# Kernel tuning notes

Hardware: AMD Instinct MI355X
Metric: run time of the kernel (lower is better)

## Reference

```python
import jax, jax.numpy as jnp
import numpy as np

N = 100000   # nodes
E = 1200000  # edges
XD = 64      # x_dim
ED = 16      # edge_attr_dim
D = 64       # hidden_size
L = 3        # n_layers
G = 512      # num graphs
C = 10       # num_class
BN_EPS = 1e-5


def setup_inputs() -> dict:
    key = jax.random.key(0)
    ks = jax.random.split(key, 30)

    def w(k, shape, scale=0.05):
        return jax.random.normal(k, shape, jnp.float32) * scale

    inp = {
        "x": jax.random.normal(ks[0], (N, XD), jnp.float32),
        "edge_index": jax.random.randint(ks[1], (2, E), 0, N),
        "batch": jnp.sort(jax.random.randint(ks[2], (N,), 0, G)),
        "edge_attr": jax.random.normal(ks[3], (E, ED), jnp.float32),
        # encoders
        "w_node": w(ks[4], (XD, D)), "b_node": jnp.zeros((D,), jnp.float32),
        "w_edge": w(ks[5], (ED, D)), "b_edge": jnp.zeros((D,), jnp.float32),
        # per-layer GINEConv params (stacked over L layers)
        "lin_w": w(ks[6], (L, D, D)), "lin_b": jnp.zeros((L, D), jnp.float32),
        "mlp1_w": w(ks[7], (L, D, D)), "mlp1_b": jnp.zeros((L, D), jnp.float32),
        "bn1_g": jnp.ones((L, D), jnp.float32), "bn1_b": jnp.zeros((L, D), jnp.float32),
        "mlp2_w": w(ks[8], (L, D, D)), "mlp2_b": jnp.zeros((L, D), jnp.float32),
        # fc_out head: MLP(D,D) -> BN -> Linear(D,C)
        "fo1_w": w(ks[9], (D, D)), "fo1_b": jnp.zeros((D,), jnp.float32),
        "fo_bn1_g": jnp.ones((D,), jnp.float32), "fo_bn1_b": jnp.zeros((D,), jnp.float32),
        "fo2_w": w(ks[10], (D, D)), "fo2_b": jnp.zeros((D,), jnp.float32),
        "fo_bn2_g": jnp.ones((D,), jnp.float32), "fo_bn2_b": jnp.zeros((D,), jnp.float32),
        "fo3_w": w(ks[11], (D, C)), "fo3_b": jnp.zeros((C,), jnp.float32),
    }
    return inp


def _bn(h, g, b):
    # training-mode BatchNorm1d: biased variance over the batch dim
    mu = h.mean(0, keepdims=True)
    var = h.var(0, keepdims=True)
    return g * (h - mu) * (var + BN_EPS) ** -0.5 + b


def reference(x, edge_index, batch, edge_attr,
              w_node, b_node, w_edge, b_edge,
              lin_w, lin_b, mlp1_w, mlp1_b, bn1_g, bn1_b, mlp2_w, mlp2_b,
              fo1_w, fo1_b, fo_bn1_g, fo_bn1_b, fo2_w, fo2_b,
              fo_bn2_g, fo_bn2_b, fo3_w, fo3_b):
    src, dst = edge_index[0], edge_index[1]  # message flows src -> dst
    h = x @ w_node + b_node                  # [N, D]
    ea0 = edge_attr @ w_edge + b_edge        # [E, D] encoded edge features
    for l in range(L):
        ea = ea0 @ lin_w[l] + lin_b[l]                      # GINEConv.lin
        m = jax.nn.relu(h[src] + ea)                        # edge messages [E, D]
        agg = jax.ops.segment_sum(m, dst, num_segments=N)   # scatter-add
        h2 = agg + h                                        # + (1 + eps) * x_r, eps = 0
        h2 = h2 @ mlp1_w[l] + mlp1_b[l]
        h2 = jax.nn.relu(_bn(h2, bn1_g[l], bn1_b[l]))
        h2 = h2 @ mlp2_w[l] + mlp2_b[l]
        h = jax.nn.relu(h2)                                 # dropout is no-op at eval
    pooled = jax.ops.segment_sum(h, batch, num_segments=G)  # global_add_pool [G, D]
    g1 = pooled @ fo1_w + fo1_b
    g1 = jax.nn.relu(_bn(g1, fo_bn1_g, fo_bn1_b))
    g1 = g1 @ fo2_w + fo2_b
    g1 = _bn(g1, fo_bn2_g, fo_bn2_b)
    return g1 @ fo3_w + fo3_b                               # logits [G, C]
```

## Files before the change

kernel.cpp:

```cpp
#include <hip/hip_runtime.h>
#include <hip/hip_fp16.h>

#define NN 100000
#define NE 1200000
#define DD 64
#define EDIM 16
#define NL 3
#define NG 512
#define NC 10
#define NB_SCAN ((NN + 255) / 256)
#define EPW 32

typedef _Float16 f16x2 __attribute__((ext_vector_type(2)));
typedef _Float16 v8h   __attribute__((ext_vector_type(8)));
typedef float    v4f   __attribute__((ext_vector_type(4)));

__device__ __forceinline__ unsigned packh2(float a, float b) {
    f16x2 v; v[0] = (_Float16)a; v[1] = (_Float16)b;
    unsigned u; __builtin_memcpy(&u, &v, 4); return u;
}
__device__ __forceinline__ float dot2f(unsigned a, unsigned b, float c) {
    f16x2 av, bv;
    __builtin_memcpy(&av, &a, 4); __builtin_memcpy(&bv, &b, 4);
#if __has_builtin(__builtin_amdgcn_fdot2)
    return __builtin_amdgcn_fdot2(av, bv, c, false);
#else
    return c + (float)av[0]*(float)bv[0] + (float)av[1]*(float)bv[1];
#endif
}

__device__ __forceinline__ void atomic_pk_add_h2(_Float16* addr, float a, float b) {
    f16x2 v; v[0] = (_Float16)a; v[1] = (_Float16)b;
#if __has_builtin(__builtin_amdgcn_global_atomic_fadd_v2f16)
    typedef __attribute__((address_space(1))) f16x2 gh2;
    __builtin_amdgcn_global_atomic_fadd_v2f16((gh2*)addr, v);
#else
    unsigned* u = (unsigned*)addr;
    unsigned old = *u, assumed;
    do {
        assumed = old;
        f16x2 w; __builtin_memcpy(&w, &assumed, 4);
        w = w + v;
        unsigned nv; __builtin_memcpy(&nv, &w, 4);
        old = atomicCAS(u, assumed, nv);
    } while (old != assumed);
#endif
}

__global__ __launch_bounds__(1024) void prep_kernel(
    const float* __restrict__ w_edge, const float* __restrict__ b_edge,
    const float* __restrict__ lin_w, const float* __restrict__ lin_b,
    unsigned* __restrict__ Wc16, float* __restrict__ bc)
{
    __shared__ float sWc[1024];
    const int l = blockIdx.x;
    const int tid = threadIdx.x;
    const float* Lw = lin_w + l * 4096;
    const int k = tid >> 6, col = tid & 63;
    float acc = 0.f;
    for (int j = 0; j < 64; ++j) acc = fmaf(w_edge[k*64 + j], Lw[j*64 + col], acc);
    sWc[k*64 + col] = acc;
    if (tid < 64) {
        float a = lin_b[l*64 + tid];
        for (int j = 0; j < 64; ++j) a = fmaf(b_edge[j], Lw[j*64 + tid], a);
        bc[l*64 + tid] = a;
    }
    __syncthreads();
    if (tid < 512) {
        const int j = tid >> 6, c = tid & 63;
        Wc16[l*512 + j*64 + c] = packh2(sWc[(2*j)*64 + c], sWc[(2*j+1)*64 + c]);
    }
}

__global__ __launch_bounds__(512) void pack_w_kernel(
    const float* __restrict__ w_node, const float* __restrict__ mlp1_w,
    const float* __restrict__ mlp2_w, v8h* __restrict__ Wpk)
{
    const int m = blockIdx.x;
    const float* W = (m == 0) ? w_node
                   : (m <= 3) ? mlp1_w + (m-1)*4096
                              : mlp2_w + (m-4)*4096;
    const int fid = threadIdx.x >> 6;
    const int l   = threadIdx.x & 63;
    const int t = fid >> 1, f = fid & 1;
    const int n  = (l & 15) + 16*t;
    const int kb = f*32 + (l >> 4)*8;
    v8h v;
    #pragma unroll
    for (int j = 0; j < 8; ++j) v[j] = (_Float16)W[(kb + j)*64 + n];
    Wpk[m*512 + fid*64 + l] = v;
}

__global__ __launch_bounds__(256) void hist_kernel(
    const int* __restrict__ dst, int* __restrict__ counts)
{
    const int e = blockIdx.x * 256 + threadIdx.x;
    if (e < NE) atomicAdd(&counts[dst[e]], 1);
}

__global__ __launch_bounds__(256) void scan_reduce_kernel(
    const int* __restrict__ counts, int* __restrict__ bsum)
{
    __shared__ int sd[256];
    const int t = threadIdx.x;
    const int idx = blockIdx.x * 256 + t;
    sd[t] = (idx < NN) ? counts[idx] : 0;
    __syncthreads();
    for (int off = 128; off > 0; off >>= 1) {
        if (t < off) sd[t] += sd[t + off];
        __syncthreads();
    }
    if (t == 0) bsum[blockIdx.x] = sd[0];
}

__global__ __launch_bounds__(512) void scan_partials_kernel(
    const int* __restrict__ bsum, int* __restrict__ bscan)
{
    __shared__ int sd[512];
    const int t = threadIdx.x;
    sd[t] = (t < NB_SCAN) ? bsum[t] : 0;
    __syncthreads();
    for (int off = 1; off < 512; off <<= 1) {
        int u = (t >= off) ? sd[t - off] : 0;
        __syncthreads();
        sd[t] += u;
        __syncthreads();
    }
    if (t < NB_SCAN) bscan[t] = (t == 0) ? 0 : sd[t - 1];
}

__global__ __launch_bounds__(256) void scan_final_kernel(
    const int* __restrict__ counts, const int* __restrict__ bscan,
    int* __restrict__ rowptr, int* __restrict__ next)
{
    __shared__ int sd[256];
    const int t = threadIdx.x;
    const int idx = blockIdx.x * 256 + t;
    const int v = (idx < NN) ? counts[idx] : 0;
    sd[t] = v;
    __syncthreads();
    for (int off = 1; off < 256; off <<= 1) {
        int u = (t >= off) ? sd[t - off] : 0;
        __syncthreads();
        sd[t] += u;
        __syncthreads();
    }
    const int excl = sd[t] - v + bscan[blockIdx.x];
    if (idx < NN) { rowptr[idx] = excl; next[idx] = excl; }
    if (idx == NN - 1) rowptr[NN] = excl + v;
}

__global__ __launch_bounds__(256) void scatter_kernel(
    const int* __restrict__ src, const int* __restrict__ dst,
    const float* __restrict__ edge_attr,
    int* __restrict__ next, int* __restrict__ csr_src, uint4* __restrict__ csr_ea)
{
    const int e = blockIdx.x * 256 + threadIdx.x;
    if (e >= NE) return;
    const float4* q = (const float4*)(edge_attr + (size_t)e * 16);
    float4 a0 = q[0], a1 = q[1], a2 = q[2], a3 = q[3];
    const int pos = atomicAdd(&next[dst[e]], 1);
    csr_src[pos] = src[e];
    uint4 A, B;
    A.x = packh2(a0.x, a0.y); A.y = packh2(a0.z, a0.w);
    A.z = packh2(a1.x, a1.y); A.w = packh2(a1.z, a1.w);
    B.x = packh2(a2.x, a2.y); B.y = packh2(a2.z, a2.w);
    B.z = packh2(a3.x, a3.y); B.w = packh2(a3.z, a3.w);
    csr_ea[(size_t)pos*2 + 0] = A;
    csr_ea[(size_t)pos*2 + 1] = B;
}

__global__ __launch_bounds__(256) void agg_edge_kernel(
    const int* __restrict__ rowptr, const int* __restrict__ csr_src,
    const uint4* __restrict__ csr_ea,
    const unsigned* __restrict__ Wc16, const float* __restrict__ bc,
    const _Float16* __restrict__ h16, _Float16* __restrict__ agg16)
{
    __shared__ uint4 sEA[4][64];
    __shared__ int   sSRC[4][32];
    const int tid  = threadIdx.x;
    const int lane = tid & 63;
    const int wv   = tid >> 6;
    const int wid  = blockIdx.x * 4 + wv;
    const int e0   = wid * EPW;

    sEA[wv][lane] = csr_ea[(size_t)e0 * 2 + lane];
    if (lane < 32) sSRC[wv][lane] = csr_src[e0 + lane];

    unsigned wq[8];
    #pragma unroll
    for (int j = 0; j < 8; ++j) wq[j] = Wc16[j*64 + lane];
    const float mb = bc[lane];

    int lo = 0;
    {
        int idx = lane * 1563; if (idx > NN) idx = NN;
        lo += (__popcll(__ballot(rowptr[idx] <= e0)) - 1) * 1563;
        idx = lo + lane * 25; if (idx > NN) idx = NN;
        lo += (__popcll(__ballot(rowptr[idx] <= e0)) - 1) * 25;
        idx = lo + lane; if (idx > NN) idx = NN;
        lo += __popcll(__ballot(rowptr[idx] <= e0)) - 1;
    }
    int cur = lo;
    int nb  = rowptr[cur + 1];
    float acc = 0.f;

    __syncthreads();

    const uint4* eaw = sEA[wv];
    const int*   srw = sSRC[wv];

    auto msg = [&](uint4 A, uint4 B, float hv) -> float {
        float m = mb;
        m = dot2f(A.x, wq[0], m); m = dot2f(A.y, wq[1], m);
        m = dot2f(A.z, wq[2], m); m = dot2f(A.w, wq[3], m);
        m = dot2f(B.x, wq[4], m); m = dot2f(B.y, wq[5], m);
        m = dot2f(B.z, wq[6], m); m = dot2f(B.w, wq[7], m);
        return fmaxf(m + hv, 0.f);
    };
    auto flush = [&](int node, float v) {
        float other = __shfl_xor(v, 1);
        if ((lane & 1) == 0)
            atomic_pk_add_h2(agg16 + (size_t)node*64 + lane, v, other);
    };
    auto adv = [&](int q) {
        flush(cur, acc); acc = 0.f;
        do { ++cur; } while (rowptr[cur + 1] <= q);
        nb = rowptr[cur + 1];
    };
    auto doGroup = [&](int g, float hv0, float hv1, float hv2, float hv3) {
        const int p = e0 + g*4;
        float m0, m1, m2, m3;
        { uint4 A = eaw[g*8+0], B = eaw[g*8+1]; m0 = msg(A, B, hv0); }
        { uint4 A = eaw[g*8+2], B = eaw[g*8+3]; m1 = msg(A, B, hv1); }
        { uint4 A = eaw[g*8+4], B = eaw[g*8+5]; m2 = msg(A, B, hv2); }
        { uint4 A = eaw[g*8+6], B = eaw[g*8+7]; m3 = msg(A, B, hv3); }
        if (p + 3 < nb) {
            acc += (m0 + m1) + (m2 + m3);
        } else {
            if (p     >= nb) adv(p);     acc += m0;
            if (p + 1 >= nb) adv(p + 1); acc += m1;
            if (p + 2 >= nb) adv(p + 2); acc += m2;
            if (p + 3 >= nb) adv(p + 3); acc += m3;
        }
    };

    _Float16 a0, a1, a2, a3, b0, b1, b2, b3;
    {
        const int4 s = *(const int4*)&srw[0];
        a0 = h16[(size_t)s.x*64 + lane]; a1 = h16[(size_t)s.y*64 + lane];
        a2 = h16[(size_t)s.z*64 + lane]; a3 = h16[(size_t)s.w*64 + lane];
    }
    #pragma unroll 1
    for (int gp = 0; gp < EPW/8; ++gp) {
        const int g0 = gp*2, g1 = g0 + 1;
        {
            const int4 s = *(const int4*)&srw[g1*4];
            b0 = h16[(size_t)s.x*64 + lane]; b1 = h16[(size_t)s.y*64 + lane];
            b2 = h16[(size_t)s.z*64 + lane]; b3 = h16[(size_t)s.w*64 + lane];
        }
        doGroup(g0, (float)a0, (float)a1, (float)a2, (float)a3);
        if (gp + 1 < EPW/8) {
            const int4 s = *(const int4*)&srw[(g1 + 1)*4];
            a0 = h16[(size_t)s.x*64 + lane]; a1 = h16[(size_t)s.y*64 + lane];
            a2 = h16[(size_t)s.z*64 + lane]; a3 = h16[(size_t)s.w*64 + lane];
        }
        doGroup(g1, (float)b0, (float)b1, (float)b2, (float)b3);
    }
    flush(cur, acc);
}

template<bool IN_HALF, bool ADD_B, bool TRANS, bool OUT_RELU, bool OUT_ACCUM, bool OUT_F32, bool OUT_HALF>
__global__ __launch_bounds__(256) void mfma_gemm_kernel(
    const float* __restrict__ in0, const _Float16* __restrict__ in16,
    const _Float16* __restrict__ in16b,
    const v8h* __restrict__ Wpk, const float* __restrict__ bias,
    const float* __restrict__ scale, const float* __restrict__ shift,
    float* __restrict__ out, _Float16* __restrict__ out16,
    float* __restrict__ bn_sum, float* __restrict__ bn_sumsq)
{
    __shared__ float sS[1024];
    __shared__ float sQ[1024];
    const int tid = threadIdx.x;
    const int wv = tid >> 6, l = tid & 63;
    const int li = l & 15, quad = l >> 4;
    const int rb = (blockIdx.x * 4 + wv) * 16;
    const bool active = (rb < NN);

    v8h Bf[8];
    #pragma unroll
    for (int i = 0; i < 8; ++i) Bf[i] = Wpk[i*64 + l];

    v4f acc[4] = {v4f{0,0,0,0}, v4f{0,0,0,0}, v4f{0,0,0,0}, v4f{0,0,0,0}};

    if (active) {
        v8h Af[2];
        if constexpr (IN_HALF) {
            const size_t off = (size_t)(rb + li)*64 + quad*8;
            Af[0] = *(const v8h*)(in16 + off);
            Af[1] = *(const v8h*)(in16 + off + 32);
            if constexpr (ADD_B) {
                Af[0] += *(const v8h*)(in16b + off);
                Af[1] += *(const v8h*)(in16b + off + 32);
            }
        } else {
            const float* arow = in0 + (size_t)(rb + li)*64 + quad*8;
            #pragma unroll
            for (int f = 0; f < 2; ++f) {
                float4 x0 = *(const float4*)(arow + f*32);
                float4 x1 = *(const float4*)(arow + f*32 + 4);
                if constexpr (TRANS) {
                    const int kb = f*32 + quad*8;
                    float4 s0 = *(const float4*)(scale + kb);
                    float4 s1 = *(const float4*)(scale + kb + 4);
                    float4 t0 = *(const float4*)(shift + kb);
                    float4 t1 = *(const float4*)(shift + kb + 4);
                    x0.x = fmaxf(fmaf(x0.x, s0.x, t0.x), 0.f);
                    x0.y = fmaxf(fmaf(x0.y, s0.y, t0.y), 0.f);
                    x0.z = fmaxf(fmaf(x0.z, s0.z, t0.z), 0.f);
                    x0.w = fmaxf(fmaf(x0.w, s0.w, t0.w), 0.f);
                    x1.x = fmaxf(fmaf(x1.x, s1.x, t1.x), 0.f);
                    x1.y = fmaxf(fmaf(x1.y, s1.y, t1.y), 0.f);
                    x1.z = fmaxf(fmaf(x1.z, s1.z, t1.z), 0.f);
                    x1.w = fmaxf(fmaf(x1.w, s1.w, t1.w), 0.f);
                }
                v8h a;
                a[0] = (_Float16)x0.x; a[1] = (_Float16)x0.y;
                a[2] = (_Float16)x0.z; a[3] = (_Float16)x0.w;
                a[4] = (_Float16)x1.x; a[5] = (_Float16)x1.y;
                a[6] = (_Float16)x1.z; a[7] = (_Float16)x1.w;
                Af[f] = a;
            }
        }
        #pragma unroll
        for (int t = 0; t < 4; ++t) {
            acc[t] = __builtin_amdgcn_mfma_f32_16x16x32_f16(Af[0], Bf[t*2+0], acc[t], 0, 0, 0);
            acc[t] = __builtin_amdgcn_mfma_f32_16x16x32_f16(Af[1], Bf[t*2+1], acc[t], 0, 0, 0);
        }
    }

    float ps[4] = {0.f, 0.f, 0.f, 0.f}, pq[4] = {0.f, 0.f, 0.f, 0.f};
    if (active) {
        #pragma unroll
        for (int t = 0; t < 4; ++t) {
            const int col = li + 16*t;
            const float bcol = bias[col];
            #pragma unroll
            for (int r = 0; r < 4; ++r) {
                const int row = rb + quad*4 + r;
                float v = acc[t][r] + bcol;
                if constexpr (OUT_ACCUM) { ps[t] += v; pq[t] += v*v; }
                if constexpr (OUT_RELU) v = fmaxf(v, 0.f);
                if constexpr (OUT_F32)  out[(size_t)row*64 + col] = v;
                if constexpr (OUT_HALF) out16[(size_t)row*64 + col] = (_Float16)v;
            }
        }
    }

    if constexpr (OUT_ACCUM) {
        #pragma unroll
        for (int t = 0; t < 4; ++t) {
            sS[wv*256 + l*4 + t] = ps[t];
            sQ[wv*256 + l*4 + t] = pq[t];
        }
        __syncthreads();
        if (tid < 64) {
            const int t = tid >> 4, li2 = tid & 15;
            float s = 0.f, q = 0.f;
            #pragma unroll
            for (int w = 0; w < 4; ++w)
                #pragma unroll
                for (int qd = 0; qd < 4; ++qd) {
                    const int idx = w*256 + (qd*16 + li2)*4 + t;
                    s += sS[idx]; q += sQ[idx];
                }
            atomicAdd(bn_sum + tid, s);
            atomicAdd(bn_sumsq + tid, q);
        }
    }
}

template<int IN_MODE, bool OUT_RELU, bool OUT_ACCUM>
__global__ __launch_bounds__(256) void gemm64_kernel(
    const float* __restrict__ in0,
    const float* __restrict__ W, const float* __restrict__ bias,
    const float* __restrict__ scale, const float* __restrict__ shift,
    float* __restrict__ out, int nrows,
    float* __restrict__ bn_sum, float* __restrict__ bn_sumsq)
{
    __shared__ __align__(16) float sIn[64*64];
    __shared__ float sRedS[512];
    __shared__ float sRedQ[512];
    const int tid = threadIdx.x;
    const int c  = tid & 31;
    const int rg = tid >> 5;
    const int r0 = blockIdx.x * 64;

    float w0[64], w1[64];
    #pragma unroll
    for (int k = 0; k < 64; ++k) { w0[k] = W[k*64 + c]; w1[k] = W[k*64 + c + 32]; }
    const float b0 = bias[c], b1 = bias[c + 32];

    for (int i = tid; i < 1024; i += 256) {
        const int r  = i >> 4;
        const int c4 = (i & 15) * 4;
        const int gr = r0 + r;
        float4 v = make_float4(0.f, 0.f, 0.f, 0.f);
        if (gr < nrows) {
            v = *(const float4*)(in0 + (size_t)gr*64 + c4);
            if constexpr (IN_MODE == 2) {
                float4 s4 = *(const float4*)(scale + c4);
                float4 h4 = *(const float4*)(shift + c4);
                v.x = fmaxf(fmaf(v.x, s4.x, h4.x), 0.f);
                v.y = fmaxf(fmaf(v.y, s4.y, h4.y), 0.f);
                v.z = fmaxf(fmaf(v.z, s4.z, h4.z), 0.f);
                v.w = fmaxf(fmaf(v.w, s4.w, h4.w), 0.f);
            }
        }
        *(float4*)(sIn + r*64 + c4) = v;
    }
    __syncthreads();

    float ps0 = 0.f, psq0 = 0.f, ps1 = 0.f, psq1 = 0.f;
    #pragma unroll
    for (int i = 0; i < 8; ++i) {
        const int r = rg + 8*i;
        float a0 = b0, a1 = b1;
        #pragma unroll
        for (int k = 0; k < 64; k += 4) {
            float4 a = *(const float4*)(sIn + r*64 + k);
            a0 = fmaf(a.x, w0[k+0], a0); a1 = fmaf(a.x, w1[k+0], a1);
            a0 = fmaf(a.y, w0[k+1], a0); a1 = fmaf(a.y, w1[k+1], a1);
            a0 = fmaf(a.z, w0[k+2], a0); a1 = fmaf(a.z, w1[k+2], a1);
            a0 = fmaf(a.w, w0[k+3], a0); a1 = fmaf(a.w, w1[k+3], a1);
        }
        const int gr = r0 + r;
        if (gr < nrows) {
            if constexpr (OUT_ACCUM) {
                ps0 += a0; psq0 += a0*a0;
                ps1 += a1; psq1 += a1*a1;
            }
            out[(size_t)gr*64 + c]      = OUT_RELU ? fmaxf(a0, 0.f) : a0;
            out[(size_t)gr*64 + c + 32] = OUT_RELU ? fmaxf(a1, 0.f) : a1;
        }
    }

    if constexpr (OUT_ACCUM) {
        sRedS[rg*64 + c]      = ps0;
        sRedS[rg*64 + c + 32] = ps1;
        sRedQ[rg*64 + c]      = psq0;
        sRedQ[rg*64 + c + 32] = psq1;
        __syncthreads();
        if (tid < 64) {
            float s = 0.f, q = 0.f;
            #pragma unroll
            for (int g = 0; g < 8; ++g) { s += sRedS[g*64 + tid]; q += sRedQ[g*64 + tid]; }
            atomicAdd(bn_sum + tid, s);
            atomicAdd(bn_sumsq + tid, q);
        }
    }
}

__global__ __launch_bounds__(64) void bn_finalize_kernel(
    const float* __restrict__ sum, const float* __restrict__ sumsq,
    const float* __restrict__ gamma, const float* __restrict__ beta,
    float inv_count, float* __restrict__ scale, float* __restrict__ shift)
{
    const int t = threadIdx.x;
    float mu  = sum[t] * inv_count;
    float var = fmaxf(sumsq[t] * inv_count - mu*mu, 0.f);
    float x = var + 1e-5f;
    float r = rsqrtf(x);
    r = r * (1.5f - 0.5f * x * r * r);
    float sc = gamma[t] * r;
    scale[t] = sc;
    shift[t] = beta[t] - mu * sc;
}

__global__ __launch_bounds__(256) void pool_kernel(
    const _Float16* __restrict__ h16, const int* __restrict__ batch,
    float* __restrict__ pooled)
{
    __shared__ float sRed[256];
    const int g = blockIdx.x;
    const int tid = threadIdx.x;
    const int lane = tid & 63, wave = tid >> 6;
    int lo = 0, hi = NN;
    while (lo < hi) { int m = (lo + hi) >> 1; if (batch[m] < g) lo = m + 1; else hi = m; }
    const int start = lo;
    hi = NN;
    while (lo < hi) { int m = (lo + hi) >> 1; if (batch[m] < g + 1) lo = m + 1; else hi = m; }
    const int end = lo;
    float acc = 0.f;
    for (int n = start + wave; n < end; n += 4) acc += (float)h16[(size_t)n*64 + lane];
    sRed[tid] = acc;
    __syncthreads();
    if (tid < 64)
        pooled[g*64 + tid] = sRed[tid] + sRed[64+tid] + sRed[128+tid] + sRed[192+tid];
}

__global__ __launch_bounds__(256) void head_final_kernel(
    const float* __restrict__ hb, const float* __restrict__ scale,
    const float* __restrict__ shift, const float* __restrict__ fo3_w,
    const float* __restrict__ fo3_b, float* __restrict__ out)
{
    const int idx = blockIdx.x * 256 + threadIdx.x;
    if (idx >= NG * NC) return;
    const int g = idx / NC, c = idx % NC;
    float acc = fo3_b[c];
    for (int k = 0; k < 64; ++k) {
        float v = fmaf(hb[g*64 + k], scale[k], shift[k]);
        acc = fmaf(v, fo3_w[k*NC + c], acc);
    }
    out[idx] = acc;
}

extern "C" void kernel_launch(void* const* d_in, const int* in_sizes, int n_in,
                              void* d_out, int out_size, void* d_ws, size_t ws_size,
                              hipStream_t stream) {
    const float* x         = (const float*)d_in[0];
    const int*   edge_index= (const int*)  d_in[1];
    const int*   batch     = (const int*)  d_in[2];
    const float* edge_attr = (const float*)d_in[3];
    const float* w_node    = (const float*)d_in[4];
    const float* b_node    = (const float*)d_in[5];
    const float* w_edge    = (const float*)d_in[6];
    const float* b_edge    = (const float*)d_in[7];
    const float* lin_w     = (const float*)d_in[8];
    const float* lin_b     = (const float*)d_in[9];
    const float* mlp1_w    = (const float*)d_in[10];
    const float* mlp1_b    = (const float*)d_in[11];
    const float* bn1_g     = (const float*)d_in[12];
    const float* bn1_b     = (const float*)d_in[13];
    const float* mlp2_w    = (const float*)d_in[14];
    const float* mlp2_b    = (const float*)d_in[15];
    const float* fo1_w     = (const float*)d_in[16];
    const float* fo1_b     = (const float*)d_in[17];
    const float* fo_bn1_g  = (const float*)d_in[18];
    const float* fo_bn1_b  = (const float*)d_in[19];
    const float* fo2_w     = (const float*)d_in[20];
    const float* fo2_b     = (const float*)d_in[21];
    const float* fo_bn2_g  = (const float*)d_in[22];
    const float* fo_bn2_b  = (const float*)d_in[23];
    const float* fo3_w     = (const float*)d_in[24];
    const float* fo3_b     = (const float*)d_in[25];
    float* out = (float*)d_out;

    char* ws = (char*)d_ws;
    float* t    = (float*)(ws);
    int* counts = (int*)t;
    int* next   = (int*)t + NN;
    int*   csr_src = (int*)(ws + 25600000);
    uint4* csr_ea  = (uint4*)(ws + 30400000);
    int* rowptr = (int*)(ws + 68800000);
    _Float16* h16   = (_Float16*)(ws + 69300000);
    _Float16* agg16 = (_Float16*)(ws + 82100000);
    float* sm   = (float*)(ws + 94900000);
    unsigned* Wc16 = (unsigned*)sm;
    float* bc       = sm + 1536;
    float* scale    = sm + 1728;
    float* shift    = sm + 1792;
    float* bn_sum   = sm + 1856;
    float* bn_sumsq = sm + 1920;
    float* pooled   = sm + 1984;
    float* ha       = sm + 34752;
    float* hb       = sm + 67520;
    int* bsum       = (int*)(sm + 100288);
    int* bscan      = bsum + 512;
    v8h* Wpk        = (v8h*)(sm + 101376);

    const int* src = edge_index;
    const int* dst = edge_index + NE;

    const int mfma_blocks  = (NN/16 + 3) / 4;
    const int edge_blocks  = (NE + 255) / 256;
    const int aggE_blocks  = NE / (EPW * 4);

    prep_kernel<<<NL, 1024, 0, stream>>>(w_edge, b_edge, lin_w, lin_b, Wc16, bc);
    pack_w_kernel<<<7, 512, 0, stream>>>(w_node, mlp1_w, mlp2_w, Wpk);

    mfma_gemm_kernel<false, false, false, false, false, false, true><<<mfma_blocks, 256, 0, stream>>>(
        x, nullptr, nullptr, Wpk, b_node, nullptr, nullptr, nullptr, h16, nullptr, nullptr);

    hipMemsetAsync(counts, 0, NN * sizeof(int), stream);
    hist_kernel<<<edge_blocks, 256, 0, stream>>>(dst, counts);
    scan_reduce_kernel<<<NB_SCAN, 256, 0, stream>>>(counts, bsum);
    scan_partials_kernel<<<1, 512, 0, stream>>>(bsum, bscan);
    scan_final_kernel<<<NB_SCAN, 256, 0, stream>>>(counts, bscan, rowptr, next);
    scatter_kernel<<<edge_blocks, 256, 0, stream>>>(
        src, dst, edge_attr, next, csr_src, csr_ea);

    for (int l = 0; l < NL; ++l) {
        hipMemsetAsync(agg16, 0, (size_t)NN * DD * sizeof(_Float16), stream);
        agg_edge_kernel<<<aggE_blocks, 256, 0, stream>>>(
            rowptr, csr_src, csr_ea, Wc16 + l*512, bc + l*64, h16, agg16);
        hipMemsetAsync(bn_sum, 0, 128 * sizeof(float), stream);
        mfma_gemm_kernel<true, true, false, false, true, true, false><<<mfma_blocks, 256, 0, stream>>>(
            nullptr, agg16, h16, Wpk + (1+l)*512, mlp1_b + l*64, nullptr, nullptr,
            t, nullptr, bn_sum, bn_sumsq);
        bn_finalize_kernel<<<1, 64, 0, stream>>>(
            bn_sum, bn_sumsq, bn1_g + l*64, bn1_b + l*64, 1.0f / NN, scale, shift);
        mfma_gemm_kernel<false, false, true, true, false, false, true><<<mfma_blocks, 256, 0, stream>>>(
            t, nullptr, nullptr, Wpk + (4+l)*512, mlp2_b + l*64, scale, shift,
            nullptr, h16, nullptr, nullptr);
    }

    pool_kernel<<<NG, 256, 0, stream>>>(h16, batch, pooled);

    hipMemsetAsync(bn_sum, 0, 128 * sizeof(float), stream);
    gemm64_kernel<0, false, true><<<NG/64, 256, 0, stream>>>(
        pooled, fo1_w, fo1_b, nullptr, nullptr, ha, NG, bn_sum, bn_sumsq);
    bn_finalize_kernel<<<1, 64, 0, stream>>>(
        bn_sum, bn_sumsq, fo_bn1_g, fo_bn1_b, 1.0f / NG, scale, shift);
    hipMemsetAsync(bn_sum, 0, 128 * sizeof(float), stream);
    gemm64_kernel<2, false, true><<<NG/64, 256, 0, stream>>>(
        ha, fo2_w, fo2_b, scale, shift, hb, NG, bn_sum, bn_sumsq);
    bn_finalize_kernel<<<1, 64, 0, stream>>>(
        bn_sum, bn_sumsq, fo_bn2_g, fo_bn2_b, 1.0f / NG, scale, shift);
    head_final_kernel<<<(NG*NC + 255)/256, 256, 0, stream>>>(
        hb, scale, shift, fo3_w, fo3_b, out);
}
```

Baseline: 751.4 us.

## Build CSR via two-pass binning by 64-node buckets to localize scatter writes

Replaces the single-pass atomic scatter into CSR with a two-stage scheme. The first pass bins packed (edge, dst-low-bits, src) records into 64-node buckets with atomics on bucket counters. The second pass, one block per bucket, assigns final positions with shared-memory atomics and writes csr_src and fp16-packed edge attributes. The aim is to turn random global writes and global atomics on 100k counters into more local, cache-friendly traffic, at the cost of an extra kernel and an 8-byte intermediate buffer per edge.

```diff
diff --git a/kernel.cpp b/kernel.cpp
--- a/kernel.cpp
+++ b/kernel.cpp
@@ -10,6 +10,7 @@
 #define NC 10
 #define NB_SCAN ((NN + 255) / 256)
 #define EPW 32
+#define NBIN ((NN + 63) / 64)
 
 typedef _Float16 f16x2 __attribute__((ext_vector_type(2)));
 typedef _Float16 v8h   __attribute__((ext_vector_type(8)));
@@ -131,7 +132,7 @@
 
 __global__ __launch_bounds__(256) void scan_final_kernel(
     const int* __restrict__ counts, const int* __restrict__ bscan,
-    int* __restrict__ rowptr, int* __restrict__ next)
+    int* __restrict__ rowptr)
 {
     __shared__ int sd[256];
     const int t = threadIdx.x;
@@ -146,28 +147,65 @@
         __syncthreads();
     }
     const int excl = sd[t] - v + bscan[blockIdx.x];
-    if (idx < NN) { rowptr[idx] = excl; next[idx] = excl; }
+    if (idx < NN) rowptr[idx] = excl;
     if (idx == NN - 1) rowptr[NN] = excl + v;
 }
 
-__global__ __launch_bounds__(256) void scatter_kernel(
+__global__ __launch_bounds__(256) void bin_init_kernel(
+    const int* __restrict__ rowptr, int* __restrict__ bin_next)
+{
+    const int b = blockIdx.x * 256 + threadIdx.x;
+    if (b < NBIN) bin_next[b] = rowptr[b << 6];
+}
+
+__global__ __launch_bounds__(256) void bin_kernel(
     const int* __restrict__ src, const int* __restrict__ dst,
-    const float* __restrict__ edge_attr,
-    int* __restrict__ next, int* __restrict__ csr_src, uint4* __restrict__ csr_ea)
+    int* __restrict__ bin_next, unsigned long long* __restrict__ bin_buf)
 {
     const int e = blockIdx.x * 256 + threadIdx.x;
     if (e >= NE) return;
-    const float4* q = (const float4*)(edge_attr + (size_t)e * 16);
-    float4 a0 = q[0], a1 = q[1], a2 = q[2], a3 = q[3];
-    const int pos = atomicAdd(&next[dst[e]], 1);
-    csr_src[pos] = src[e];
-    uint4 A, B;
-    A.x = packh2(a0.x, a0.y); A.y = packh2(a0.z, a0.w);
-    A.z = packh2(a1.x, a1.y); A.w = packh2(a1.z, a1.w);
-    B.x = packh2(a2.x, a2.y); B.y = packh2(a2.z, a2.w);
-    B.z = packh2(a3.x, a3.y); B.w = packh2(a3.z, a3.w);
-    csr_ea[(size_t)pos*2 + 0] = A;
-    csr_ea[(size_t)pos*2 + 1] = B;
+    const int s = src[e], d = dst[e];
+    const unsigned long long v =
+        ((unsigned long long)e << 23) | ((unsigned long long)(d & 63) << 17) | (unsigned)s;
+    const int pos = atomicAdd(&bin_next[d >> 6], 1);
+    bin_buf[pos] = v;
+}
+
+__global__ __launch_bounds__(256) void order_pack_kernel(
+    const int* __restrict__ rowptr, const unsigned long long* __restrict__ bin_buf,
+    const float* __restrict__ edge_attr,
+    int* __restrict__ csr_src, uint4* __restrict__ csr_ea)
+{
+    __shared__ int lnext[65];
+    const int b = blockIdx.x;
+    const int tid = threadIdx.x;
+    const int node0 = b << 6;
+    if (tid < 65) {
+        int idx = node0 + tid; if (idx > NN) idx = NN;
+        lnext[tid] = rowptr[idx];
+    }
+    __syncthreads();
+    const int base = lnext[0];
+    int end_idx = node0 + 64; if (end_idx > NN) end_idx = NN;
+    const int cnt = rowptr[end_idx] - base;
+
+    for (int k = tid; k < cnt; k += 256) {
+        const unsigned long long v = bin_buf[base + k];
+        const int s  = (int)(v & 0x1FFFF);
+        const int d6 = (int)((v >> 17) & 63);
+        const int e  = (int)(v >> 23);
+        const int pos = atomicAdd(&lnext[d6], 1);
+        csr_src[pos] = s;
+        const float4* q = (const float4*)(edge_attr + (size_t)e * 16);
+        float4 a0 = q[0], a1 = q[1], a2 = q[2], a3 = q[3];
+        uint4 A, B;
+        A.x = packh2(a0.x, a0.y); A.y = packh2(a0.z, a0.w);
+        A.z = packh2(a1.x, a1.y); A.w = packh2(a1.z, a1.w);
+        B.x = packh2(a2.x, a2.y); B.y = packh2(a2.z, a2.w);
+        B.z = packh2(a3.x, a3.y); B.w = packh2(a3.z, a3.w);
+        csr_ea[(size_t)pos*2 + 0] = A;
+        csr_ea[(size_t)pos*2 + 1] = B;
+    }
 }
 
 __global__ __launch_bounds__(256) void agg_edge_kernel(
@@ -549,7 +587,8 @@
     char* ws = (char*)d_ws;
     float* t    = (float*)(ws);
     int* counts = (int*)t;
-    int* next   = (int*)t + NN;
+    unsigned long long* bin_buf =
+        (unsigned long long*)(ws + 800000);
     int*   csr_src = (int*)(ws + 25600000);
     uint4* csr_ea  = (uint4*)(ws + 30400000);
     int* rowptr = (int*)(ws + 68800000);
@@ -568,6 +607,7 @@
     int* bsum       = (int*)(sm + 100288);
     int* bscan      = bsum + 512;
     v8h* Wpk        = (v8h*)(sm + 101376);
+    int* bin_next   = (int*)(sm + 101376 + 14336);
 
     const int* src = edge_index;
     const int* dst = edge_index + NE;
@@ -586,9 +626,10 @@
     hist_kernel<<<edge_blocks, 256, 0, stream>>>(dst, counts);
     scan_reduce_kernel<<<NB_SCAN, 256, 0, stream>>>(counts, bsum);
     scan_partials_kernel<<<1, 512, 0, stream>>>(bsum, bscan);
-    scan_final_kernel<<<NB_SCAN, 256, 0, stream>>>(counts, bscan, rowptr, next);
-    scatter_kernel<<<edge_blocks, 256, 0, stream>>>(
-        src, dst, edge_attr, next, csr_src, csr_ea);
+    scan_final_kernel<<<NB_SCAN, 256, 0, stream>>>(counts, bscan, rowptr);
+    bin_init_kernel<<<(NBIN + 255)/256, 256, 0, stream>>>(rowptr, bin_next);
+    bin_kernel<<<edge_blocks, 256, 0, stream>>>(src, dst, bin_next, bin_buf);
+    order_pack_kernel<<<NBIN, 256, 0, stream>>>(rowptr, bin_buf, edge_attr, csr_src, csr_ea);
 
     for (int l = 0; l < NL; ++l) {
         hipMemsetAsync(agg16, 0, (size_t)NN * DD * sizeof(_Float16), stream);
```

Measured after the change: 909.9 us. 1.21x slower.

## Fold BN finalize into consumer kernels and fuse pooling into last GEMM

Applied to the files above, without the earlier changes.

Removes the separate bn_finalize kernels: each consumer GEMM or head kernel now computes BN scale and shift from the accumulated sums into shared memory. The per-call BN sum memsets are replaced by a single up-front memset of a combined buffer that holds per-stage statistics and the pooled array. The final layer's second GEMM writes relu outputs straight into pooled through atomics, with a wave-level reduction when all 16 rows belong to one graph, so the h16 write and the pool kernel are dropped. This cuts about a dozen small launches and one pass over the node features, at the cost of float atomics into pooled whose summation order is nondeterministic.

```diff
diff --git a/kernel.cpp b/kernel.cpp
--- a/kernel.cpp
+++ b/kernel.cpp
@@ -45,6 +45,17 @@
         old = atomicCAS(u, assumed, nv);
     } while (old != assumed);
 #endif
+}
+
+__device__ __forceinline__ void bn_sc_sh(float s, float q, float g, float b,
+                                         float invc, float& sc, float& sh) {
+    float mu  = s * invc;
+    float var = fmaxf(q * invc - mu * mu, 0.f);
+    float x = var + 1e-5f;
+    float r = rsqrtf(x);
+    r = r * (1.5f - 0.5f * x * r * r);
+    sc = g * r;
+    sh = b - mu * sc;
 }
 
 __global__ __launch_bounds__(1024) void prep_kernel(
@@ -270,22 +281,34 @@
     flush(cur, acc);
 }
 
-template<bool IN_HALF, bool ADD_B, bool TRANS, bool OUT_RELU, bool OUT_ACCUM, bool OUT_F32, bool OUT_HALF>
+template<bool IN_HALF, bool ADD_B, bool TRANS, bool OUT_RELU, bool OUT_ACCUM,
+         bool OUT_F32, bool OUT_HALF, bool OUT_POOL>
 __global__ __launch_bounds__(256) void mfma_gemm_kernel(
     const float* __restrict__ in0, const _Float16* __restrict__ in16,
     const _Float16* __restrict__ in16b,
     const v8h* __restrict__ Wpk, const float* __restrict__ bias,
-    const float* __restrict__ scale, const float* __restrict__ shift,
+    const float* __restrict__ bni_sum, const float* __restrict__ bni_sumsq,
+    const float* __restrict__ bni_g, const float* __restrict__ bni_b,
+    float bni_invc,
     float* __restrict__ out, _Float16* __restrict__ out16,
-    float* __restrict__ bn_sum, float* __restrict__ bn_sumsq)
+    float* __restrict__ bn_sum, float* __restrict__ bn_sumsq,
+    const int* __restrict__ batch, float* __restrict__ pooled)
 {
     __shared__ float sS[1024];
     __shared__ float sQ[1024];
+    __shared__ float sSc[64], sSh[64];
     const int tid = threadIdx.x;
     const int wv = tid >> 6, l = tid & 63;
     const int li = l & 15, quad = l >> 4;
     const int rb = (blockIdx.x * 4 + wv) * 16;
     const bool active = (rb < NN);
+
+    if constexpr (TRANS) {
+        if (tid < 64)
+            bn_sc_sh(bni_sum[tid], bni_sumsq[tid], bni_g[tid], bni_b[tid],
+                     bni_invc, sSc[tid], sSh[tid]);
+        __syncthreads();
+    }
 
     v8h Bf[8];
     #pragma unroll
@@ -311,10 +334,10 @@
                 float4 x1 = *(const float4*)(arow + f*32 + 4);
                 if constexpr (TRANS) {
                     const int kb = f*32 + quad*8;
-                    float4 s0 = *(const float4*)(scale + kb);
-                    float4 s1 = *(const float4*)(scale + kb + 4);
-                    float4 t0 = *(const float4*)(shift + kb);
-                    float4 t1 = *(const float4*)(shift + kb + 4);
+                    float4 s0 = *(const float4*)(sSc + kb);
+                    float4 s1 = *(const float4*)(sSc + kb + 4);
+                    float4 t0 = *(const float4*)(sSh + kb);
+                    float4 t1 = *(const float4*)(sSh + kb + 4);
                     x0.x = fmaxf(fmaf(x0.x, s0.x, t0.x), 0.f);
                     x0.y = fmaxf(fmaf(x0.y, s0.y, t0.y), 0.f);
                     x0.z = fmaxf(fmaf(x0.z, s0.z, t0.z), 0.f);
@@ -339,43 +362,77 @@
         }
     }
 
-    float ps[4] = {0.f, 0.f, 0.f, 0.f}, pq[4] = {0.f, 0.f, 0.f, 0.f};
-    if (active) {
-        #pragma unroll
-        for (int t = 0; t < 4; ++t) {
-            const int col = li + 16*t;
-            const float bcol = bias[col];
+    if constexpr (OUT_F32 || OUT_HALF || OUT_ACCUM) {
+        float ps[4] = {0.f, 0.f, 0.f, 0.f}, pq[4] = {0.f, 0.f, 0.f, 0.f};
+        if (active) {
             #pragma unroll
-            for (int r = 0; r < 4; ++r) {
-                const int row = rb + quad*4 + r;
-                float v = acc[t][r] + bcol;
-                if constexpr (OUT_ACCUM) { ps[t] += v; pq[t] += v*v; }
-                if constexpr (OUT_RELU) v = fmaxf(v, 0.f);
-                if constexpr (OUT_F32)  out[(size_t)row*64 + col] = v;
-                if constexpr (OUT_HALF) out16[(size_t)row*64 + col] = (_Float16)v;
-            }
-        }
-    }
-
-    if constexpr (OUT_ACCUM) {
-        #pragma unroll
-        for (int t = 0; t < 4; ++t) {
-            sS[wv*256 + l*4 + t] = ps[t];
-            sQ[wv*256 + l*4 + t] = pq[t];
-        }
-        __syncthreads();
-        if (tid < 64) {
-            const int t = tid >> 4, li2 = tid & 15;
-            float s = 0.f, q = 0.f;
+            for (int t = 0; t < 4; ++t) {
+                const int col = li + 16*t;
+                const float bcol = bias[col];
+                #pragma unroll
+                for (int r = 0; r < 4; ++r) {
+                    const int row = rb + quad*4 + r;
+                    float v = acc[t][r] + bcol;
+                    if constexpr (OUT_ACCUM) { ps[t] += v; pq[t] += v*v; }
+                    if constexpr (OUT_RELU) v = fmaxf(v, 0.f);
+                    if constexpr (OUT_F32)  out[(size_t)row*64 + col] = v;
+                    if constexpr (OUT_HALF) out16[(size_t)row*64 + col] = (_Float16)v;
+                }
+            }
+        }
+        if constexpr (OUT_ACCUM) {
             #pragma unroll
-            for (int w = 0; w < 4; ++w)
+            for (int t = 0; t < 4; ++t) {
+                sS[wv*256 + l*4 + t] = ps[t];
+                sQ[wv*256 + l*4 + t] = pq[t];
+            }
+            __syncthreads();
+            if (tid < 64) {
+                const int t = tid >> 4, li2 = tid & 15;
+                float s = 0.f, q = 0.f;
                 #pragma unroll
-                for (int qd = 0; qd < 4; ++qd) {
-                    const int idx = w*256 + (qd*16 + li2)*4 + t;
-                    s += sS[idx]; q += sQ[idx];
+                for (int w = 0; w < 4; ++w)
+                    #pragma unroll
+                    for (int qd = 0; qd < 4; ++qd) {
+                        const int idx = w*256 + (qd*16 + li2)*4 + t;
+                        s += sS[idx]; q += sQ[idx];
+                    }
+                atomicAdd(bn_sum + tid, s);
+                atomicAdd(bn_sumsq + tid, q);
+            }
+        }
+    }
+
+    if constexpr (OUT_POOL) {
+        if (active) {
+            const int b0  = batch[rb];
+            const int b15 = batch[rb + 15];
+            if (b0 == b15) {
+                #pragma unroll
+                for (int t = 0; t < 4; ++t) {
+                    const int col = li + 16*t;
+                    const float bcol = bias[col];
+                    float s = 0.f;
+                    #pragma unroll
+                    for (int r = 0; r < 4; ++r)
+                        s += fmaxf(acc[t][r] + bcol, 0.f);
+                    s += __shfl_xor(s, 16);
+                    s += __shfl_xor(s, 32);
+                    if (quad == 0) atomicAdd(&pooled[b0*64 + col], s);
                 }
-            atomicAdd(bn_sum + tid, s);
-            atomicAdd(bn_sumsq + tid, q);
+            } else {
+                #pragma unroll
+                for (int t = 0; t < 4; ++t) {
+                    const int col = li + 16*t;
+                    const float bcol = bias[col];
+                    #pragma unroll
+                    for (int r = 0; r < 4; ++r) {
+                        const int row = rb + quad*4 + r;
+                        const float v = fmaxf(acc[t][r] + bcol, 0.f);
+                        atomicAdd(&pooled[batch[row]*64 + col], v);
+                    }
+                }
+            }
         }
     }
 }
@@ -384,17 +441,27 @@
 __global__ __launch_bounds__(256) void gemm64_kernel(
     const float* __restrict__ in0,
     const float* __restrict__ W, const float* __restrict__ bias,
-    const float* __restrict__ scale, const float* __restrict__ shift,
+    const float* __restrict__ bni_sum, const float* __restrict__ bni_sumsq,
+    const float* __restrict__ bni_g, const float* __restrict__ bni_b,
+    float bni_invc,
     float* __restrict__ out, int nrows,
     float* __restrict__ bn_sum, float* __restrict__ bn_sumsq)
 {
     __shared__ __align__(16) float sIn[64*64];
     __shared__ float sRedS[512];
     __shared__ float sRedQ[512];
+    __shared__ __align__(16) float sSc[64], sSh[64];
     const int tid = threadIdx.x;
     const int c  = tid & 31;
     const int rg = tid >> 5;
     const int r0 = blockIdx.x * 64;
+
+    if constexpr (IN_MODE == 2) {
+        if (tid < 64)
+            bn_sc_sh(bni_sum[tid], bni_sumsq[tid], bni_g[tid], bni_b[tid],
+                     bni_invc, sSc[tid], sSh[tid]);
+        __syncthreads();
+    }
 
     float w0[64], w1[64];
     #pragma unroll
@@ -409,8 +476,8 @@
         if (gr < nrows) {
             v = *(const float4*)(in0 + (size_t)gr*64 + c4);
             if constexpr (IN_MODE == 2) {
-                float4 s4 = *(const float4*)(scale + c4);
-                float4 h4 = *(const float4*)(shift + c4);
+                float4 s4 = *(const float4*)(sSc + c4);
+                float4 h4 = *(const float4*)(sSh + c4);
                 v.x = fmaxf(fmaf(v.x, s4.x, h4.x), 0.f);
                 v.y = fmaxf(fmaf(v.y, s4.y, h4.y), 0.f);
                 v.z = fmaxf(fmaf(v.z, s4.z, h4.z), 0.f);
@@ -461,55 +528,26 @@
     }
 }
 
-__global__ __launch_bounds__(64) void bn_finalize_kernel(
-    const float* __restrict__ sum, const float* __restrict__ sumsq,
-    const float* __restrict__ gamma, const float* __restrict__ beta,
-    float inv_count, float* __restrict__ scale, float* __restrict__ shift)
-{
-    const int t = threadIdx.x;
-    float mu  = sum[t] * inv_count;
-    float var = fmaxf(sumsq[t] * inv_count - mu*mu, 0.f);
-    float x = var + 1e-5f;
-    float r = rsqrtf(x);
-    r = r * (1.5f - 0.5f * x * r * r);
-    float sc = gamma[t] * r;
-    scale[t] = sc;
-    shift[t] = beta[t] - mu * sc;
-}
-
-__global__ __launch_bounds__(256) void pool_kernel(
-    const _Float16* __restrict__ h16, const int* __restrict__ batch,
-    float* __restrict__ pooled)
-{
-    __shared__ float sRed[256];
-    const int g = blockIdx.x;
+__global__ __launch_bounds__(256) void head_final_kernel(
+    const float* __restrict__ hb,
+    const float* __restrict__ bni_sum, const float* __restrict__ bni_sumsq,
+    const float* __restrict__ bni_g, const float* __restrict__ bni_b,
+    float bni_invc,
+    const float* __restrict__ fo3_w, const float* __restrict__ fo3_b,
+    float* __restrict__ out)
+{
+    __shared__ float sSc[64], sSh[64];
     const int tid = threadIdx.x;
-    const int lane = tid & 63, wave = tid >> 6;
-    int lo = 0, hi = NN;
-    while (lo < hi) { int m = (lo + hi) >> 1; if (batch[m] < g) lo = m + 1; else hi = m; }
-    const int start = lo;
-    hi = NN;
-    while (lo < hi) { int m = (lo + hi) >> 1; if (batch[m] < g + 1) lo = m + 1; else hi = m; }
-    const int end = lo;
-    float acc = 0.f;
-    for (int n = start + wave; n < end; n += 4) acc += (float)h16[(size_t)n*64 + lane];
-    sRed[tid] = acc;
+    if (tid < 64)
+        bn_sc_sh(bni_sum[tid], bni_sumsq[tid], bni_g[tid], bni_b[tid],
+                 bni_invc, sSc[tid], sSh[tid]);
     __syncthreads();
-    if (tid < 64)
-        pooled[g*64 + tid] = sRed[tid] + sRed[64+tid] + sRed[128+tid] + sRed[192+tid];
-}
-
-__global__ __launch_bounds__(256) void head_final_kernel(
-    const float* __restrict__ hb, const float* __restrict__ scale,
-    const float* __restrict__ shift, const float* __restrict__ fo3_w,
-    const float* __restrict__ fo3_b, float* __restrict__ out)
-{
-    const int idx = blockIdx.x * 256 + threadIdx.x;
+    const int idx = blockIdx.x * 256 + tid;
     if (idx >= NG * NC) return;
     const int g = idx / NC, c = idx % NC;
     float acc = fo3_b[c];
     for (int k = 0; k < 64; ++k) {
-        float v = fmaf(hb[g*64 + k], scale[k], shift[k]);
+        float v = fmaf(hb[g*64 + k], sSc[k], sSh[k]);
         acc = fmaf(v, fo3_w[k*NC + c], acc);
     }
     out[idx] = acc;
@@ -558,16 +596,13 @@
     float* sm   = (float*)(ws + 94900000);
     unsigned* Wc16 = (unsigned*)sm;
     float* bc       = sm + 1536;
-    float* scale    = sm + 1728;
-    float* shift    = sm + 1792;
-    float* bn_sum   = sm + 1856;
-    float* bn_sumsq = sm + 1920;
-    float* pooled   = sm + 1984;
-    float* ha       = sm + 34752;
-    float* hb       = sm + 67520;
-    int* bsum       = (int*)(sm + 100288);
+    float* bnbuf    = sm + 1728;
+    float* pooled   = sm + 2368;
+    float* ha       = sm + 35136;
+    float* hb       = sm + 67904;
+    int* bsum       = (int*)(sm + 100672);
     int* bscan      = bsum + 512;
-    v8h* Wpk        = (v8h*)(sm + 101376);
+    v8h* Wpk        = (v8h*)(sm + 101696);
 
     const int* src = edge_index;
     const int* dst = edge_index + NE;
@@ -579,10 +614,14 @@
     prep_kernel<<<NL, 1024, 0, stream>>>(w_edge, b_edge, lin_w, lin_b, Wc16, bc);
     pack_w_kernel<<<7, 512, 0, stream>>>(w_node, mlp1_w, mlp2_w, Wpk);
 
-    mfma_gemm_kernel<false, false, false, false, false, false, true><<<mfma_blocks, 256, 0, stream>>>(
-        x, nullptr, nullptr, Wpk, b_node, nullptr, nullptr, nullptr, h16, nullptr, nullptr);
+    mfma_gemm_kernel<false, false, false, false, false, false, true, false>
+        <<<mfma_blocks, 256, 0, stream>>>(
+        x, nullptr, nullptr, Wpk, b_node,
+        nullptr, nullptr, nullptr, nullptr, 0.f,
+        nullptr, h16, nullptr, nullptr, nullptr, nullptr);
 
     hipMemsetAsync(counts, 0, NN * sizeof(int), stream);
+    hipMemsetAsync(bnbuf, 0, (640 + 32768) * sizeof(float), stream);
     hist_kernel<<<edge_blocks, 256, 0, stream>>>(dst, counts);
     scan_reduce_kernel<<<NB_SCAN, 256, 0, stream>>>(counts, bsum);
     scan_partials_kernel<<<1, 512, 0, stream>>>(bsum, bscan);
@@ -591,32 +630,41 @@
         src, dst, edge_attr, next, csr_src, csr_ea);
 
     for (int l = 0; l < NL; ++l) {
+        float* bnL = bnbuf + l * 128;
         hipMemsetAsync(agg16, 0, (size_t)NN * DD * sizeof(_Float16), stream);
         agg_edge_kernel<<<aggE_blocks, 256, 0, stream>>>(
             rowptr, csr_src, csr_ea, Wc16 + l*512, bc + l*64, h16, agg16);
-        hipMemsetAsync(bn_sum, 0, 128 * sizeof(float), stream);
-        mfma_gemm_kernel<true, true, false, false, true, true, false><<<mfma_blocks, 256, 0, stream>>>(
-            nullptr, agg16, h16, Wpk + (1+l)*512, mlp1_b + l*64, nullptr, nullptr,
-            t, nullptr, bn_sum, bn_sumsq);
-        bn_finalize_kernel<<<1, 64, 0, stream>>>(
-            bn_sum, bn_sumsq, bn1_g + l*64, bn1_b + l*64, 1.0f / NN, scale, shift);
-        mfma_gemm_kernel<false, false, true, true, false, false, true><<<mfma_blocks, 256, 0, stream>>>(
-            t, nullptr, nullptr, Wpk + (4+l)*512, mlp2_b + l*64, scale, shift,
-            nullptr, h16, nullptr, nullptr);
-    }
-
-    pool_kernel<<<NG, 256, 0, stream>>>(h16, batch, pooled);
-
-    hipMemsetAsync(bn_sum, 0, 128 * sizeof(float), stream);
+        mfma_gemm_kernel<true, true, false, false, true, true, false, false>
+            <<<mfma_blocks, 256, 0, stream>>>(
+            nullptr, agg16, h16, Wpk + (1+l)*512, mlp1_b + l*64,
+            nullptr, nullptr, nullptr, nullptr, 0.f,
+            t, nullptr, bnL, bnL + 64, nullptr, nullptr);
+        if (l < NL - 1) {
+            mfma_gemm_kernel<false, false, true, true, false, false, true, false>
+                <<<mfma_blocks, 256, 0, stream>>>(
+                t, nullptr, nullptr, Wpk + (4+l)*512, mlp2_b + l*64,
+                bnL, bnL + 64, bn1_g + l*64, bn1_b + l*64, 1.0f / NN,
+                nullptr, h16, nullptr, nullptr, nullptr, nullptr);
+        } else {
+            mfma_gemm_kernel<false, false, true, true, false, false, false, true>
+                <<<mfma_blocks, 256, 0, stream>>>(
+                t, nullptr, nullptr, Wpk + (4+l)*512, mlp2_b + l*64,
+                bnL, bnL + 64, bn1_g + l*64, bn1_b + l*64, 1.0f / NN,
+                nullptr, nullptr, nullptr, nullptr, batch, pooled);
+        }
+    }
+
+    float* bnH1 = bnbuf + 3 * 128;
+    float* bnH2 = bnbuf + 4 * 128;
     gemm64_kernel<0, false, true><<<NG/64, 256, 0, stream>>>(
-        pooled, fo1_w, fo1_b, nullptr, nullptr, ha, NG, bn_sum, bn_sumsq);
-    bn_finalize_kernel<<<1, 64, 0, stream>>>(
-        bn_sum, bn_sumsq, fo_bn1_g, fo_bn1_b, 1.0f / NG, scale, shift);
-    hipMemsetAsync(bn_sum, 0, 128 * sizeof(float), stream);
+        pooled, fo1_w, fo1_b,
+        nullptr, nullptr, nullptr, nullptr, 0.f,
+        ha, NG, bnH1, bnH1 + 64);
     gemm64_kernel<2, false, true><<<NG/64, 256, 0, stream>>>(
-        ha, fo2_w, fo2_b, scale, shift, hb, NG, bn_sum, bn_sumsq);
-    bn_finalize_kernel<<<1, 64, 0, stream>>>(
-        bn_sum, bn_sumsq, fo_bn2_g, fo_bn2_b, 1.0f / NG, scale, shift);
+        ha, fo2_w, fo2_b,
+        bnH1, bnH1 + 64, fo_bn1_g, fo_bn1_b, 1.0f / NG,
+        hb, NG, bnH2, bnH2 + 64);
     head_final_kernel<<<(NG*NC + 255)/256, 256, 0, stream>>>(
-        hb, scale, shift, fo3_w, fo3_b, out);
-}
+        hb, bnH2, bnH2 + 64, fo_bn2_g, fo_bn2_b, 1.0f / NG,
+        fo3_w, fo3_b, out);
+}
```

After: 716.9 us. 1.05x faster.
